# Performance work log

Measured on AMD Instinct MI355X. Metric: run time of the kernel, lower is better.

## Reference

```python
import jax, jax.numpy as jnp
import numpy as np

T, B, D, H = 512, 64, 1024, 1024

def setup_inputs() -> dict:
    key = jax.random.key(0)
    k1, k2, k3, k4, k5 = jax.random.split(key, 5)
    scale_x = np.sqrt(6.0) / np.sqrt(D + 4 * H)
    scale_h = np.sqrt(6.0) / np.sqrt(H + 4 * H)
    x_data = jax.random.normal(k1, (T, B, D), dtype=jnp.float32)
    # binary mask (1 = valid token), as used for variable-length sequences
    x_mask = (jax.random.uniform(k2, (T, B)) < 0.9).astype(jnp.float32)
    Wx = jax.random.uniform(k3, (4 * H, D), minval=-scale_x, maxval=scale_x, dtype=jnp.float32)
    bx = jax.random.uniform(k4, (4 * H,), minval=-scale_x, maxval=scale_x, dtype=jnp.float32)
    Wh = jax.random.uniform(k5, (4 * H, H), minval=-scale_h, maxval=scale_h, dtype=jnp.float32)
    return {"x_data": x_data, "x_mask": x_mask, "Wx": Wx, "bx": bx, "Wh": Wh}

def _lstm_forward(x_data, x_mask, Wx, bx, Wh):
    # Precompute input projections for all timesteps in one GEMM: [T,B,4H]
    xg = jnp.einsum('tbd,gd->tbg', x_data, Wx) + bx
    Hh = Wh.shape[1]

    def step(carry, inp):
        htm, ctm = carry
        xg_t, m_t = inp  # [B,4H], [B]
        gates = xg_t + htm @ Wh.T
        ig, fg, og, ct = jnp.split(gates, 4, axis=1)
        ig = jax.nn.sigmoid(ig)
        fg = jax.nn.sigmoid(fg)
        og = jax.nn.sigmoid(og)
        ct = jnp.tanh(ct)
        ct = fg * ctm + ig * ct
        ht = og * jnp.tanh(ct)
        m = m_t[:, None]
        ct = ct * m + ctm * (1.0 - m)
        ht = ht * m + htm * (1.0 - m)
        return (ht, ct), ht

    h0 = jnp.zeros((x_data.shape[1], Hh), dtype=x_data.dtype)
    c0 = jnp.zeros((x_data.shape[1], Hh), dtype=x_data.dtype)
    _, output = jax.lax.scan(step, (h0, c0), (xg, x_mask))
    return output  # [T,B,H]

def reference(x_data, x_mask, Wx, bx, Wh):
    return _lstm_forward(x_data, x_mask, Wx, bx, Wh)
```

## Files before the change

### kernel.cpp

```cpp
#include <hip/hip_runtime.h>
#include <hip/hip_bf16.h>

using f32x4  = __attribute__((ext_vector_type(4))) float;
using bf16x8 = __attribute__((ext_vector_type(8))) __bf16;
using u64    = unsigned long long;

#define T_DIM 512
#define B_DIM 64
#define D_DIM 1024
#define H_DIM 1024
#define G_DIM 4096
#define NWG   128
#define WGT   512

__global__ void f32_to_bf16_kernel(const float* __restrict__ src,
                                   __bf16* __restrict__ dst, long n) {
    long i = ((long)blockIdx.x * blockDim.x + threadIdx.x) * 8;
    if (i + 8 <= n) {
        f32x4 a = *(const f32x4*)(src + i);
        f32x4 b = *(const f32x4*)(src + i + 4);
        bf16x8 o;
        o[0] = (__bf16)a[0]; o[1] = (__bf16)a[1];
        o[2] = (__bf16)a[2]; o[3] = (__bf16)a[3];
        o[4] = (__bf16)b[0]; o[5] = (__bf16)b[1];
        o[6] = (__bf16)b[2]; o[7] = (__bf16)b[3];
        *(bf16x8*)(dst + i) = o;
    }
}

#define BM 128
#define BN 128
#define BK 64

__global__ __launch_bounds__(256) void gemm_xg_kernel(
    const __bf16* __restrict__ A,
    const __bf16* __restrict__ W,
    const float* __restrict__ bias,
    float* __restrict__ C,
    int M)
{
    (void)M;
    __shared__ __bf16 sA[BM * BK];
    __shared__ __bf16 sB[BN * BK];

    const int tid = threadIdx.x;
    const int wv  = tid >> 6;
    const int l   = tid & 63;
    const int wy  = wv >> 1, wx = wv & 1;
    const int bm  = blockIdx.y * BM;
    const int bn  = blockIdx.x * BN;
    const int n   = l & 15;
    const int q   = l >> 4;

    const int srow  = l >> 3;
    const int skoff = (l & 7) * 8;

    f32x4 acc[4][4];
    #pragma unroll
    for (int mt = 0; mt < 4; ++mt)
        #pragma unroll
        for (int nt = 0; nt < 4; ++nt)
            acc[mt][nt] = (f32x4){0.f, 0.f, 0.f, 0.f};

    for (int kt = 0; kt < D_DIM / BK; ++kt) {
        const int k0 = kt * BK;
        #pragma unroll
        for (int j = 0; j < 4; ++j) {
            const int rbase = (j * 4 + wv) * 8;
            const __bf16* ga = A + (long)(bm + rbase + srow) * D_DIM + k0 + skoff;
            const __bf16* gb = W + (long)(bn + rbase + srow) * D_DIM + k0 + skoff;
            __builtin_amdgcn_global_load_lds(
                (const __attribute__((address_space(1))) void*)ga,
                (__attribute__((address_space(3))) void*)(sA + rbase * BK), 16, 0, 0);
            __builtin_amdgcn_global_load_lds(
                (const __attribute__((address_space(1))) void*)gb,
                (__attribute__((address_space(3))) void*)(sB + rbase * BK), 16, 0, 0);
        }
        __syncthreads();

        #pragma unroll
        for (int ks = 0; ks < 2; ++ks) {
            bf16x8 af[4], bfr[4];
            #pragma unroll
            for (int mt = 0; mt < 4; ++mt) {
                int row = wy * 64 + mt * 16 + n;
                af[mt] = *(const bf16x8*)(sA + row * BK + ks * 32 + q * 8);
            }
            #pragma unroll
            for (int nt = 0; nt < 4; ++nt) {
                int col = wx * 64 + nt * 16 + n;
                bfr[nt] = *(const bf16x8*)(sB + col * BK + ks * 32 + q * 8);
            }
            #pragma unroll
            for (int mt = 0; mt < 4; ++mt)
                #pragma unroll
                for (int nt = 0; nt < 4; ++nt)
                    acc[mt][nt] = __builtin_amdgcn_mfma_f32_16x16x32_bf16(
                        af[mt], bfr[nt], acc[mt][nt], 0, 0, 0);
        }
        __syncthreads();
    }

    #pragma unroll
    for (int nt = 0; nt < 4; ++nt) {
        int col = bn + wx * 64 + nt * 16 + n;
        float b = bias[col];
        #pragma unroll
        for (int mt = 0; mt < 4; ++mt) {
            #pragma unroll
            for (int r = 0; r < 4; ++r) {
                int row = bm + wy * 64 + mt * 16 + q * 4 + r;
                C[(long)row * G_DIM + col] = acc[mt][nt][r] + b;
            }
        }
    }
}

__device__ __forceinline__ float fast_tanh(float x) {
    return 1.0f - 2.0f / (__expf(2.0f * x) + 1.0f);
}

__device__ __forceinline__ void grid_barrier(unsigned* __restrict__ flags,
                                             unsigned target, int tid,
                                             int wgid, int rblk) {
    __syncthreads();
    if (tid == 0)
        __hip_atomic_store(&flags[wgid * 16], target, __ATOMIC_RELAXED,
                           __HIP_MEMORY_SCOPE_AGENT);
    if (tid < 64) {
        const unsigned* fp = &flags[(rblk * 32 + (tid & 31)) * 16];
        for (;;) {
            unsigned v = __hip_atomic_load(fp, __ATOMIC_RELAXED,
                                           __HIP_MEMORY_SCOPE_AGENT);
            if (__all(v >= target)) break;
            __builtin_amdgcn_s_sleep(1);
        }
    }
    __syncthreads();
    __atomic_signal_fence(__ATOMIC_ACQUIRE);
}

__global__ __launch_bounds__(WGT)
__attribute__((amdgpu_waves_per_eu(2, 2)))
void lstm_scan_kernel(
    const __bf16* __restrict__ Whb,
    const float* __restrict__ xg,
    const float* __restrict__ mask,
    float* __restrict__ cst,
    __bf16* __restrict__ hbuf,
    float* __restrict__ out,
    unsigned* __restrict__ flags,
    int t0, int tc)
{
    __shared__ __align__(16) char shh[32768];
    __shared__ float sg[8][16 * 17];

    const int tid  = threadIdx.x;
    const int wgid = blockIdx.x;
    const int rblk = wgid >> 5;
    const int ublk = wgid & 31;
    const int wv   = tid >> 6;
    const int l    = tid & 63;
    const int n    = l & 15;
    const int q    = l >> 4;

    const int colg = ((n >> 2) << 10) + ublk * 32 + wv * 4 + (n & 3);

    bf16x8 breg[32];
    #pragma unroll
    for (int kk = 0; kk < 32; ++kk)
        breg[kk] = *(const bf16x8*)(Whb + (long)colg * H_DIM + kk * 32 + q * 8);

    const int rloc = l >> 2;
    const int ui   = l & 3;
    const int grow = rblk * 16 + rloc;
    const int ucol = ublk * 32 + wv * 4 + ui;

    float c_r, h_r;
    if (t0 == 0) { c_r = 0.0f; h_r = 0.0f; }
    else {
        c_r = cst[grow * H_DIM + ucol];
        h_r = out[((long)(t0 - 1) * B_DIM + grow) * H_DIM + ucol];
    }

    float xc0, xc1, xc2, xc3, mkc;
    {
        const float* xr = xg + (long)grow * G_DIM + ucol;
        xc0 = xr[0]; xc1 = xr[H_DIM]; xc2 = xr[2 * H_DIM]; xc3 = xr[3 * H_DIM];
        mkc = mask[t0 * B_DIM + grow];
    }

    const int srow_lo = (l >> 3);
    const int sv      = l & 7;
    const int sq      = (l >> 1) & 3;
    const int sb      = (l & 1) * 8;

    for (int t = 0; t < tc; ++t) {
        #pragma unroll
        for (int kk = 0; kk < 32; ++kk)
            asm volatile("" : "+v"(breg[kk]));

        const int gt = t0 + t;
        const __bf16* hread = hbuf + (long)(gt & 1) * (B_DIM * H_DIM);
        __bf16* hwrite = hbuf + (long)((gt + 1) & 1) * (B_DIM * H_DIM);
        const u64* h64 = (const u64*)hread;

        u64 hold[8];
        #pragma unroll
        for (int j = 0; j < 4; ++j) {
            const int kk = wv * 4 + j;
            hold[j * 2]     = __hip_atomic_load(
                h64 + (long)(rblk * 16 + srow_lo) * 256 + kk * 8 + sv,
                __ATOMIC_RELAXED, __HIP_MEMORY_SCOPE_AGENT);
            hold[j * 2 + 1] = __hip_atomic_load(
                h64 + (long)(rblk * 16 + 8 + srow_lo) * 256 + kk * 8 + sv,
                __ATOMIC_RELAXED, __HIP_MEMORY_SCOPE_AGENT);
        }
        #pragma unroll
        for (int j = 0; j < 4; ++j) {
            const int kk = wv * 4 + j;
            *(u64*)(shh + kk * 1024 + sq * 256 + srow_lo * 16 + sb)       = hold[j * 2];
            *(u64*)(shh + kk * 1024 + sq * 256 + (8 + srow_lo) * 16 + sb) = hold[j * 2 + 1];
        }
        __syncthreads();

        f32x4 ac0 = {0.f,0.f,0.f,0.f}, ac1 = {0.f,0.f,0.f,0.f};
        #pragma unroll
        for (int kk = 0; kk < 32; kk += 2) {
            bf16x8 f0 = *(const bf16x8*)(shh + (kk + 0) * 1024 + q * 256 + n * 16);
            bf16x8 f1 = *(const bf16x8*)(shh + (kk + 1) * 1024 + q * 256 + n * 16);
            ac0 = __builtin_amdgcn_mfma_f32_16x16x32_bf16(f0, breg[kk + 0], ac0, 0, 0, 0);
            ac1 = __builtin_amdgcn_mfma_f32_16x16x32_bf16(f1, breg[kk + 1], ac1, 0, 0, 0);
        }
        f32x4 acc = ac0 + ac1;

        #pragma unroll
        for (int r = 0; r < 4; ++r)
            sg[wv][(q * 4 + r) * 17 + n] = acc[r];

        float ig = xc0 + sg[wv][rloc * 17 + 0  + ui];
        float fg = xc1 + sg[wv][rloc * 17 + 4  + ui];
        float og = xc2 + sg[wv][rloc * 17 + 8  + ui];
        float gg = xc3 + sg[wv][rloc * 17 + 12 + ui];

        float i_s = 1.0f / (1.0f + __expf(-ig));
        float f_s = 1.0f / (1.0f + __expf(-fg));
        float o_s = 1.0f / (1.0f + __expf(-og));
        float g_t = fast_tanh(gg);
        float c_new = f_s * c_r + i_s * g_t;
        float h_new = o_s * fast_tanh(c_new);
        float c_f = mkc * c_new + (1.0f - mkc) * c_r;
        float h_f = mkc * h_new + (1.0f - mkc) * h_r;
        c_r = c_f;
        h_r = h_f;

        const int base = l & ~3;
        float v0 = __shfl(h_f, base + 0);
        float v1 = __shfl(h_f, base + 1);
        float v2 = __shfl(h_f, base + 2);
        float v3 = __shfl(h_f, base + 3);
        if (ui == 0) {
            f32x4 ov = {v0, v1, v2, v3};
            *(f32x4*)(out + ((long)gt * B_DIM + grow) * H_DIM + ublk * 32 + wv * 4) = ov;
            unsigned short b0 = __builtin_bit_cast(unsigned short, (__bf16)v0);
            unsigned short b1 = __builtin_bit_cast(unsigned short, (__bf16)v1);
            unsigned short b2 = __builtin_bit_cast(unsigned short, (__bf16)v2);
            unsigned short b3 = __builtin_bit_cast(unsigned short, (__bf16)v3);
            u64 pk = (u64)b0 | ((u64)b1 << 16) | ((u64)b2 << 32) | ((u64)b3 << 48);
            u64* dp = (u64*)((unsigned short*)hwrite +
                             (long)grow * H_DIM + ublk * 32 + wv * 4);
            __hip_atomic_store(dp, pk, __ATOMIC_RELAXED, __HIP_MEMORY_SCOPE_AGENT);
        }

        if (t == tc - 1) cst[grow * H_DIM + ucol] = c_f;

        if (t + 1 < tc) {
            const float* xr = xg + ((long)(t + 1) * B_DIM + grow) * G_DIM + ucol;
            xc0 = xr[0]; xc1 = xr[H_DIM]; xc2 = xr[2 * H_DIM]; xc3 = xr[3 * H_DIM];
            mkc = mask[(gt + 1) * B_DIM + grow];
        }

        grid_barrier(flags, (unsigned)(gt + 1), tid, wgid, rblk);
    }
}

extern "C" void kernel_launch(void* const* d_in, const int* in_sizes, int n_in,
                              void* d_out, int out_size, void* d_ws, size_t ws_size,
                              hipStream_t stream)
{
    (void)in_sizes; (void)n_in; (void)out_size;
    const float* x     = (const float*)d_in[0];
    const float* xmask = (const float*)d_in[1];
    const float* Wx    = (const float*)d_in[2];
    const float* bx    = (const float*)d_in[3];
    const float* Wh    = (const float*)d_in[4];
    float* out = (float*)d_out;

    char* ws = (char*)d_ws;
    __bf16*   Whb   = (__bf16*)(ws);
    __bf16*   Wxb   = (__bf16*)(ws + 8388608);
    __bf16*   hb    = (__bf16*)(ws + 16777216);
    float*    cst   = (float*)(ws + 16777216 + 262144);
    unsigned* flags = (unsigned*)(ws + 16777216 + 524288);
    char* dyn = ws + 16777216 + 1048576;

    long avail = (long)ws_size - (16777216L + 1048576L);
    const long per_t = (long)B_DIM * D_DIM * 2 + (long)B_DIM * G_DIM * 4;
    long Tc = avail > 0 ? avail / per_t : 2;
    if (Tc > T_DIM) Tc = T_DIM;
    Tc &= ~1L;
    if (Tc < 2) Tc = 2;

    __bf16* xb = (__bf16*)dyn;
    float*  xg = (float*)(dyn + Tc * (long)B_DIM * D_DIM * 2);

    hipMemsetAsync(ws + 16777216, 0, 1048576, stream);

    {
        long nw = (long)G_DIM * D_DIM;
        int nb = (int)(nw / 8 / 256);
        f32_to_bf16_kernel<<<nb, 256, 0, stream>>>(Wx, Wxb, nw);
        f32_to_bf16_kernel<<<nb, 256, 0, stream>>>(Wh, Whb, nw);
    }

    for (int t0 = 0; t0 < T_DIM; t0 += (int)Tc) {
        int tc = (int)((T_DIM - t0 < Tc) ? (long)(T_DIM - t0) : Tc);

        long nx = (long)tc * B_DIM * D_DIM;
        f32_to_bf16_kernel<<<(int)(nx / 8 / 256), 256, 0, stream>>>(
            x + (long)t0 * B_DIM * D_DIM, xb, nx);

        dim3 gg(G_DIM / BN, (tc * B_DIM) / BM);
        gemm_xg_kernel<<<gg, 256, 0, stream>>>(xb, Wxb, bx, xg, tc * B_DIM);

        const __bf16* Whb_a = Whb;
        const float*  xg_a  = xg;
        const float*  mask_a = xmask;
        float*  cst_a = cst;
        __bf16* hb_a  = hb;
        float*  out_a = out;
        unsigned* fl_a = flags;
        int t0_a = t0, tc_a = tc;
        void* args[] = {(void*)&Whb_a, (void*)&xg_a, (void*)&mask_a,
                        (void*)&cst_a, (void*)&hb_a, (void*)&out_a,
                        (void*)&fl_a, (void*)&t0_a, (void*)&tc_a};
        hipLaunchCooperativeKernel((void*)lstm_scan_kernel, dim3(NWG), dim3(WGT),
                                   args, 0, stream);
    }
}
```

Measured before the change: 2.560 ms.

## Replace grid barrier with epoch-tagged hidden state polled directly by consumers

```diff
diff --git a/kernel.cpp b/kernel.cpp
--- a/kernel.cpp
+++ b/kernel.cpp
@@ -4,6 +4,7 @@
 using f32x4  = __attribute__((ext_vector_type(4))) float;
 using bf16x8 = __attribute__((ext_vector_type(8))) __bf16;
 using u64    = unsigned long long;
+using u32    = unsigned int;
 
 #define T_DIM 512
 #define B_DIM 64
@@ -120,26 +121,6 @@
     return 1.0f - 2.0f / (__expf(2.0f * x) + 1.0f);
 }
 
-__device__ __forceinline__ void grid_barrier(unsigned* __restrict__ flags,
-                                             unsigned target, int tid,
-                                             int wgid, int rblk) {
-    __syncthreads();
-    if (tid == 0)
-        __hip_atomic_store(&flags[wgid * 16], target, __ATOMIC_RELAXED,
-                           __HIP_MEMORY_SCOPE_AGENT);
-    if (tid < 64) {
-        const unsigned* fp = &flags[(rblk * 32 + (tid & 31)) * 16];
-        for (;;) {
-            unsigned v = __hip_atomic_load(fp, __ATOMIC_RELAXED,
-                                           __HIP_MEMORY_SCOPE_AGENT);
-            if (__all(v >= target)) break;
-            __builtin_amdgcn_s_sleep(1);
-        }
-    }
-    __syncthreads();
-    __atomic_signal_fence(__ATOMIC_ACQUIRE);
-}
-
 __global__ __launch_bounds__(WGT)
 __attribute__((amdgpu_waves_per_eu(2, 2)))
 void lstm_scan_kernel(
@@ -147,9 +128,8 @@
     const float* __restrict__ xg,
     const float* __restrict__ mask,
     float* __restrict__ cst,
-    __bf16* __restrict__ hbuf,
+    u32* __restrict__ hbuf,
     float* __restrict__ out,
-    unsigned* __restrict__ flags,
     int t0, int tc)
 {
     __shared__ __align__(16) char shh[32768];
@@ -176,6 +156,11 @@
     const int grow = rblk * 16 + rloc;
     const int ucol = ublk * 32 + wv * 4 + ui;
 
+    const int srow   = (wv & 1) * 8 + (l >> 3);
+    const int pb     = (wv >> 1) * 64 + (l & 7);
+    const long grow_s = (long)(rblk * 16 + srow);
+    const int lds_off = ((l >> 1) & 3) * 256 + srow * 16 + (l & 1) * 8;
+
     float c_r, h_r;
     if (t0 == 0) { c_r = 0.0f; h_r = 0.0f; }
     else {
@@ -190,37 +175,47 @@
         mkc = mask[t0 * B_DIM + grow];
     }
 
-    const int srow_lo = (l >> 3);
-    const int sv      = l & 7;
-    const int sq      = (l >> 1) & 3;
-    const int sb      = (l & 1) * 8;
-
     for (int t = 0; t < tc; ++t) {
-        #pragma unroll
-        for (int kk = 0; kk < 32; ++kk)
-            asm volatile("" : "+v"(breg[kk]));
-
         const int gt = t0 + t;
-        const __bf16* hread = hbuf + (long)(gt & 1) * (B_DIM * H_DIM);
-        __bf16* hwrite = hbuf + (long)((gt + 1) & 1) * (B_DIM * H_DIM);
-        const u64* h64 = (const u64*)hread;
-
-        u64 hold[8];
-        #pragma unroll
-        for (int j = 0; j < 4; ++j) {
-            const int kk = wv * 4 + j;
-            hold[j * 2]     = __hip_atomic_load(
-                h64 + (long)(rblk * 16 + srow_lo) * 256 + kk * 8 + sv,
-                __ATOMIC_RELAXED, __HIP_MEMORY_SCOPE_AGENT);
-            hold[j * 2 + 1] = __hip_atomic_load(
-                h64 + (long)(rblk * 16 + 8 + srow_lo) * 256 + kk * 8 + sv,
-                __ATOMIC_RELAXED, __HIP_MEMORY_SCOPE_AGENT);
-        }
-        #pragma unroll
-        for (int j = 0; j < 4; ++j) {
-            const int kk = wv * 4 + j;
-            *(u64*)(shh + kk * 1024 + sq * 256 + srow_lo * 16 + sb)       = hold[j * 2];
-            *(u64*)(shh + kk * 1024 + sq * 256 + (8 + srow_lo) * 16 + sb) = hold[j * 2 + 1];
+        const u32 ep  = (u32)gt & 0xFFFFu;
+        const u32 ep1 = (u32)(gt + 1) & 0xFFFFu;
+        const u64 et64 = ((u64)ep << 16) | ((u64)ep << 48);
+        const u32* hr = hbuf + (long)(gt & 1) * (B_DIM * H_DIM);
+        u32* hw = hbuf + (long)((gt + 1) & 1) * (B_DIM * H_DIM);
+
+        u64 lo[8], hi[8];
+        #pragma unroll
+        for (int s = 0; s < 8; ++s) {
+            const u32* p = hr + grow_s * H_DIM + (pb + s * 8) * 4;
+            lo[s] = __hip_atomic_load((const u64*)p,     __ATOMIC_RELAXED, __HIP_MEMORY_SCOPE_AGENT);
+            hi[s] = __hip_atomic_load((const u64*)p + 1, __ATOMIC_RELAXED, __HIP_MEMORY_SCOPE_AGENT);
+        }
+        unsigned pend = 0xFFu;
+        while (pend) {
+            unsigned np = 0;
+            #pragma unroll
+            for (int s = 0; s < 8; ++s) {
+                if (pend & (1u << s)) {
+                    if ((((lo[s] ^ et64) | (hi[s] ^ et64)) & 0xFFFF0000FFFF0000ull) != 0ull) {
+                        const u32* p = hr + grow_s * H_DIM + (pb + s * 8) * 4;
+                        lo[s] = __hip_atomic_load((const u64*)p,     __ATOMIC_RELAXED, __HIP_MEMORY_SCOPE_AGENT);
+                        hi[s] = __hip_atomic_load((const u64*)p + 1, __ATOMIC_RELAXED, __HIP_MEMORY_SCOPE_AGENT);
+                        np |= 1u << s;
+                    }
+                }
+            }
+            pend = np;
+            if (pend) __builtin_amdgcn_s_sleep(1);
+        }
+
+        #pragma unroll
+        for (int s = 0; s < 8; ++s) {
+            u32 w0 = (u32)lo[s], w1 = (u32)(lo[s] >> 32);
+            u32 w2 = (u32)hi[s], w3 = (u32)(hi[s] >> 32);
+            u64 pk = (u64)(unsigned short)w0 | ((u64)(unsigned short)w1 << 16)
+                   | ((u64)(unsigned short)w2 << 32) | ((u64)(unsigned short)w3 << 48);
+            const int kk = (wv >> 1) * 8 + s;
+            *(u64*)(shh + kk * 1024 + lds_off) = pk;
         }
         __syncthreads();
 
@@ -260,16 +255,17 @@
         float v2 = __shfl(h_f, base + 2);
         float v3 = __shfl(h_f, base + 3);
         if (ui == 0) {
+            u32 t0s = (ep1 << 16) | (u32)__builtin_bit_cast(unsigned short, (__bf16)v0);
+            u32 t1s = (ep1 << 16) | (u32)__builtin_bit_cast(unsigned short, (__bf16)v1);
+            u32 t2s = (ep1 << 16) | (u32)__builtin_bit_cast(unsigned short, (__bf16)v2);
+            u32 t3s = (ep1 << 16) | (u32)__builtin_bit_cast(unsigned short, (__bf16)v3);
+            u64 pk0 = (u64)t0s | ((u64)t1s << 32);
+            u64 pk1 = (u64)t2s | ((u64)t3s << 32);
+            u64* dp = (u64*)(hw + (long)grow * H_DIM + ublk * 32 + wv * 4);
+            __hip_atomic_store(dp,     pk0, __ATOMIC_RELAXED, __HIP_MEMORY_SCOPE_AGENT);
+            __hip_atomic_store(dp + 1, pk1, __ATOMIC_RELAXED, __HIP_MEMORY_SCOPE_AGENT);
             f32x4 ov = {v0, v1, v2, v3};
             *(f32x4*)(out + ((long)gt * B_DIM + grow) * H_DIM + ublk * 32 + wv * 4) = ov;
-            unsigned short b0 = __builtin_bit_cast(unsigned short, (__bf16)v0);
-            unsigned short b1 = __builtin_bit_cast(unsigned short, (__bf16)v1);
-            unsigned short b2 = __builtin_bit_cast(unsigned short, (__bf16)v2);
-            unsigned short b3 = __builtin_bit_cast(unsigned short, (__bf16)v3);
-            u64 pk = (u64)b0 | ((u64)b1 << 16) | ((u64)b2 << 32) | ((u64)b3 << 48);
-            u64* dp = (u64*)((unsigned short*)hwrite +
-                             (long)grow * H_DIM + ublk * 32 + wv * 4);
-            __hip_atomic_store(dp, pk, __ATOMIC_RELAXED, __HIP_MEMORY_SCOPE_AGENT);
         }
 
         if (t == tc - 1) cst[grow * H_DIM + ucol] = c_f;
@@ -280,7 +276,7 @@
             mkc = mask[(gt + 1) * B_DIM + grow];
         }
 
-        grid_barrier(flags, (unsigned)(gt + 1), tid, wgid, rblk);
+        __syncthreads();
     }
 }
 
@@ -297,11 +293,10 @@
     float* out = (float*)d_out;
 
     char* ws = (char*)d_ws;
-    __bf16*   Whb   = (__bf16*)(ws);
-    __bf16*   Wxb   = (__bf16*)(ws + 8388608);
-    __bf16*   hb    = (__bf16*)(ws + 16777216);
-    float*    cst   = (float*)(ws + 16777216 + 262144);
-    unsigned* flags = (unsigned*)(ws + 16777216 + 524288);
+    __bf16* Whb = (__bf16*)(ws);
+    __bf16* Wxb = (__bf16*)(ws + 8388608);
+    u32*    hb  = (u32*)(ws + 16777216);
+    float*  cst = (float*)(ws + 16777216 + 524288);
     char* dyn = ws + 16777216 + 1048576;
 
     long avail = (long)ws_size - (16777216L + 1048576L);
@@ -337,13 +332,12 @@
         const float*  xg_a  = xg;
         const float*  mask_a = xmask;
         float*  cst_a = cst;
-        __bf16* hb_a  = hb;
+        u32*    hb_a  = hb;
         float*  out_a = out;
-        unsigned* fl_a = flags;
         int t0_a = t0, tc_a = tc;
         void* args[] = {(void*)&Whb_a, (void*)&xg_a, (void*)&mask_a,
                         (void*)&cst_a, (void*)&hb_a, (void*)&out_a,
-                        (void*)&fl_a, (void*)&t0_a, (void*)&tc_a};
+                        (void*)&t0_a, (void*)&tc_a};
         hipLaunchCooperativeKernel((void*)lstm_scan_kernel, dim3(NWG), dim3(WGT),
                                    args, 0, stream);
     }
```

After: 3.313 ms. 29.4% more time.
